# Kernel optimization log

Measured on AMD Instinct MI355X. Metric: run time of the kernel, lower is better.

## Reference

```python
import jax, jax.numpy as jnp
import numpy as np

IGNORE_INDEX = -100


def setup_inputs() -> dict:
    key = jax.random.key(0)
    k1, k2, k3 = jax.random.split(key, 3)
    BT, H, V = 2048, 2048, 128000
    x = jax.random.normal(k1, (BT, H), dtype=jnp.float32)
    weight = jax.random.normal(k2, (V, H), dtype=jnp.float32) * (1.0 / np.sqrt(H))
    target = jax.random.randint(k3, (BT,), 0, V, dtype=jnp.int64)
    return {"x": x, "weight": weight, "target": target}


def reference(x, weight, target):
    # Fused linear + cross-entropy forward (reduction='mean').
    # logits: [BT, V], accumulated in fp32 like the helion kernel.
    logits = jnp.einsum("bh,vh->bv", x.astype(jnp.float32), weight.astype(jnp.float32))
    lse = jax.nn.logsumexp(logits, axis=-1)  # [BT]
    target_logit = jnp.take_along_axis(logits, target[:, None], axis=-1)[:, 0]
    valid = (target != IGNORE_INDEX)
    nll = (lse - target_logit) * valid.astype(jnp.float32)  # [BT]
    n_non_ignore = valid.sum().astype(jnp.float32)
    loss = nll.sum() / n_non_ignore
    return loss.astype(x.dtype), lse
```

## Files before the change

kernel.cpp:

```cpp
#include <hip/hip_runtime.h>
#include <hip/hip_bf16.h>


typedef __bf16 bf16x8 __attribute__((ext_vector_type(8)));
typedef float f32x4  __attribute__((ext_vector_type(4)));
typedef float f32x16 __attribute__((ext_vector_type(16)));

#define BM 128
#define BN 128
#define BK 32
#define LDK 40

__device__ __forceinline__ unsigned pkbf(float a, float b) {
  __hip_bfloat162 h = __float22bfloat162_rn(float2{a, b});
  unsigned r;
  __builtin_memcpy(&r, &h, 4);
  return r;
}

__device__ __forceinline__ void gl16(const void* g, const void* l) {
  using GP = const unsigned __attribute__((address_space(1)))*;
  using LP = unsigned __attribute__((address_space(3)))*;
  __builtin_amdgcn_global_load_lds((GP)(unsigned long long)g,
                                   (LP)(unsigned)(unsigned long long)l, 16, 0, 0);
}

__global__ __launch_bounds__(256)
void k_cvt256(const float* __restrict__ src, __bf16* __restrict__ dst, int H, int NT)
{
  const int bid = blockIdx.x;
  const int kt = bid % NT;
  const int r = threadIdx.x;
  const float* s = src + (size_t)((bid / NT) * 256 + r) * H + kt * 64;
  __bf16* d = dst + (size_t)bid * 16384;
  #pragma unroll
  for (int j = 0; j < 8; ++j) {
    float4 f0 = ((const float4*)s)[2 * j];
    float4 f1 = ((const float4*)s)[2 * j + 1];
    uint4 p;
    p.x = pkbf(f0.x, f0.y); p.y = pkbf(f0.z, f0.w);
    p.z = pkbf(f1.x, f1.y); p.w = pkbf(f1.z, f1.w);
    *(uint4*)(d + (j >> 2) * 8192 + (j & 3) * 2048 + r * 8) = p;
  }
}

__global__ __launch_bounds__(256)
void k_tgt(const float* __restrict__ x, const float* __restrict__ w,
           const int* __restrict__ tgt, float* __restrict__ ws_t, int H)
{
  const int row  = blockIdx.x * 4 + (threadIdx.x >> 6);
  const int lane = threadIdx.x & 63;
  const int tv = tgt[row];
  if (tv == -100) { if (lane == 0) ws_t[row] = 0.f; return; }
  const float* xr = x + (size_t)row * H;
  const float* wr = w + (size_t)tv * H;
  float acc = 0.f;
  for (int j = lane * 4; j < H; j += 256) {
    float4 a = *(const float4*)(xr + j);
    float4 b = *(const float4*)(wr + j);
    acc += a.x * b.x + a.y * b.y + a.z * b.z + a.w * b.w;
  }
  #pragma unroll
  for (int m = 1; m < 64; m <<= 1) acc += __shfl_xor(acc, m, 64);
  if (lane == 0) ws_t[row] = acc;
}

#define VM4 asm volatile("s_waitcnt vmcnt(4)" ::: "memory");
#define VM0 asm volatile("s_waitcnt vmcnt(0)" ::: "memory");
#define NOVM
#define MEMFENCE asm volatile("" ::: "memory");

#define SLOT(SL, SLN, BCUR, BNXT, DO_ST, ST_S, DO_RA, VMW, DO_BAR)              \
  {                                                                             \
    _Pragma("unroll")                                                           \
    for (int m = 0; m < 4; ++m)                                                 \
      a1[m] = *(const bf16x8*)&As[SL][kcoff + (arow + (m + 4) * 16) * 8];       \
    __builtin_amdgcn_s_setprio(1);                                              \
    _Pragma("unroll")                                                           \
    for (int m = 0; m < 4; ++m)                                                 \
      _Pragma("unroll")                                                         \
      for (int n = 0; n < 4; ++n)                                               \
        acc[m][n] = __builtin_amdgcn_mfma_f32_16x16x32_bf16(a0[m], BCUR[n],     \
                                                            acc[m][n], 0, 0, 0);\
    __builtin_amdgcn_s_setprio(0);                                              \
    if (DO_ST) stage_slot(ST_S);                                                \
    VMW                                                                         \
    if (DO_BAR) { __builtin_amdgcn_s_barrier(); MEMFENCE }                      \
    if (DO_RA) {                                                                \
      _Pragma("unroll")                                                         \
      for (int m = 0; m < 4; ++m)                                               \
        a0[m] = *(const bf16x8*)&As[SLN][kcoff + (arow + m * 16) * 8];          \
      _Pragma("unroll")                                                         \
      for (int n = 0; n < 4; ++n)                                               \
        BNXT[n] = *(const bf16x8*)&Bs[SLN][kcoff + (bcol + n * 16) * 8];        \
    }                                                                           \
    __builtin_amdgcn_s_setprio(1);                                              \
    _Pragma("unroll")                                                           \
    for (int m = 0; m < 4; ++m)                                                 \
      _Pragma("unroll")                                                         \
      for (int n = 0; n < 4; ++n)                                               \
        acc[m + 4][n] = __builtin_amdgcn_mfma_f32_16x16x32_bf16(a1[m], BCUR[n], \
                                                         acc[m + 4][n], 0, 0, 0);\
    __builtin_amdgcn_s_setprio(0);                                              \
  }

__global__ __launch_bounds__(512, 2)
void k_gemm16(const __bf16* __restrict__ xb, const __bf16* __restrict__ wb,
              float* __restrict__ ws_m, float* __restrict__ ws_s,
              int NT, int NCB, int ROWB)
{
  __shared__ __bf16 As[4][8192];
  __shared__ __bf16 Bs[4][8192];

  int wg = blockIdx.x;
  const int nwg = gridDim.x;
  if ((nwg & 7) == 0) wg = (wg & 7) * (nwg >> 3) + (wg >> 3);
  const int rowb = wg % ROWB;
  const int cb   = wg / ROWB;
  const int row0 = rowb * 256;

  const int t    = threadIdx.x;
  const int lane = t & 63;
  const int wv   = t >> 6;
  const int wr   = wv >> 2;
  const int wc   = wv & 3;

  const int kcoff = (lane >> 4) * 2048;
  const int arow  = wr * 128 + (lane & 15);
  const int bcol  = wc * 64 + (lane & 15);

  const __bf16* ga = xb + (size_t)(rowb * NT) * 16384;
  const __bf16* gb = wb + (size_t)(cb * NT) * 16384;

  auto stage_slot = [&](int s) {
    const int ph = s & 3;
    const size_t off = (size_t)(s >> 1) * 16384 + (size_t)(s & 1) * 8192
                     + wv * 512 + lane * 8;
    const __bf16* a = ga + off;
    const __bf16* b = gb + off;
    gl16(a,        &As[ph][wv * 512]);
    gl16(a + 4096, &As[ph][4096 + wv * 512]);
    gl16(b,        &Bs[ph][wv * 512]);
    gl16(b + 4096, &Bs[ph][4096 + wv * 512]);
  };

  const int S = NT * 2;

  stage_slot(0); stage_slot(1);
  VM4
  __builtin_amdgcn_s_barrier();
  MEMFENCE

  f32x4 acc[8][4] = {};
  bf16x8 a0[4], a1[4], b0[4], b1[4];
  #pragma unroll
  for (int m = 0; m < 4; ++m)
    a0[m] = *(const bf16x8*)&As[0][kcoff + (arow + m * 16) * 8];
  #pragma unroll
  for (int n = 0; n < 4; ++n)
    b0[n] = *(const bf16x8*)&Bs[0][kcoff + (bcol + n * 16) * 8];

  for (int g = 0; g < (S - 4) / 4; ++g) {
    const int j0 = g * 4;
    SLOT(0, 1, b0, b1, true, j0 + 2, true, VM4, true)
    SLOT(1, 2, b1, b0, true, j0 + 3, true, VM4, true)
    SLOT(2, 3, b0, b1, true, j0 + 4, true, VM4, true)
    SLOT(3, 0, b1, b0, true, j0 + 5, true, VM4, true)
  }
  SLOT(0, 1, b0, b1, true,  S - 2, true,  VM4, true)
  SLOT(1, 2, b1, b0, true,  S - 1, true,  VM4, true)
  SLOT(2, 3, b0, b1, false, 0,     true,  VM0, true)
  SLOT(3, 0, b1, b0, false, 0,     false, NOVM, false)

  __syncthreads();

  float* redM = (float*)&As[0][0];
  float* redS = redM + 1024;
  const int g4 = (lane >> 4) * 4;
  #pragma unroll
  for (int m = 0; m < 8; ++m) {
    #pragma unroll
    for (int r = 0; r < 4; ++r) {
      const int rl = wr * 128 + m * 16 + g4 + r;
      float mx = fmaxf(fmaxf(acc[m][0][r], acc[m][1][r]),
                       fmaxf(acc[m][2][r], acc[m][3][r]));
      #pragma unroll
      for (int sh = 1; sh < 16; sh <<= 1) mx = fmaxf(mx, __shfl_xor(mx, sh, 64));
      float sv = 0.f;
      #pragma unroll
      for (int n = 0; n < 4; ++n) sv += expf(acc[m][n][r] - mx);
      #pragma unroll
      for (int sh = 1; sh < 16; sh <<= 1) sv += __shfl_xor(sv, sh, 64);
      if ((lane & 15) == 0) { redM[wc * 256 + rl] = mx; redS[wc * 256 + rl] = sv; }
    }
  }
  __syncthreads();
  if (t < 256) {
    const float m0 = redM[t], m1 = redM[256 + t], m2 = redM[512 + t], m3 = redM[768 + t];
    float M = fmaxf(fmaxf(m0, m1), fmaxf(m2, m3));
    float S2 = redS[t] * expf(m0 - M) + redS[256 + t] * expf(m1 - M)
             + redS[512 + t] * expf(m2 - M) + redS[768 + t] * expf(m3 - M);
    const int grow = row0 + t;
    ws_m[(size_t)grow * NCB + cb] = M;
    ws_s[(size_t)grow * NCB + cb] = S2;
  }
}

__global__ __launch_bounds__(256, 2)
void k_gemm_lse(const float* __restrict__ x, const float* __restrict__ w,
                const int* __restrict__ tgt,
                float* __restrict__ ws_m, float* __restrict__ ws_s,
                float* __restrict__ ws_t,
                int H, int NCB, int ROWB)
{
  __shared__ unsigned short As[2][BM * LDK];
  __shared__ unsigned short Bs[2][BN * LDK];

  const int bid  = blockIdx.x;
  const int rowb = bid % ROWB;
  const int cb   = bid / ROWB;
  const int row0 = rowb * BM;
  const int col0 = cb * BN;

  const int t    = threadIdx.x;
  const int lane = t & 63;
  const int wv   = t >> 6;
  const int sr = t >> 1;
  const int sk = (t & 1) * 16;

  const float* xa = x + (size_t)(row0 + sr) * H + sk;
  const float* wb = w + (size_t)(col0 + sr) * H + sk;

  float4 ra[4], rb[4];
  #pragma unroll
  for (int i = 0; i < 4; ++i) {
    ra[i] = *(const float4*)(xa + i * 4);
    rb[i] = *(const float4*)(wb + i * 4);
  }

  auto stage = [&](int buf) {
    uint4 p0, p1;
    p0.x = pkbf(ra[0].x, ra[0].y); p0.y = pkbf(ra[0].z, ra[0].w);
    p0.z = pkbf(ra[1].x, ra[1].y); p0.w = pkbf(ra[1].z, ra[1].w);
    p1.x = pkbf(ra[2].x, ra[2].y); p1.y = pkbf(ra[2].z, ra[2].w);
    p1.z = pkbf(ra[3].x, ra[3].y); p1.w = pkbf(ra[3].z, ra[3].w);
    *(uint4*)&As[buf][sr * LDK + sk]     = p0;
    *(uint4*)&As[buf][sr * LDK + sk + 8] = p1;
    p0.x = pkbf(rb[0].x, rb[0].y); p0.y = pkbf(rb[0].z, rb[0].w);
    p0.z = pkbf(rb[1].x, rb[1].y); p0.w = pkbf(rb[1].z, rb[1].w);
    p1.x = pkbf(rb[2].x, rb[2].y); p1.y = pkbf(rb[2].z, rb[2].w);
    p1.z = pkbf(rb[3].x, rb[3].y); p1.w = pkbf(rb[3].z, rb[3].w);
    *(uint4*)&Bs[buf][sr * LDK + sk]     = p0;
    *(uint4*)&Bs[buf][sr * LDK + sk + 8] = p1;
  };

  stage(0);
  __syncthreads();

  f32x16 acc[4] = {};
  const int rlo = lane & 31;
  const int hi  = lane >> 5;
  const int NT  = H / BK;
  int cur = 0;

  for (int kt = 0; kt < NT; ++kt) {
    const bool pf = (kt + 1 < NT);
    if (pf) {
      xa += BK; wb += BK;
      #pragma unroll
      for (int i = 0; i < 4; ++i) {
        ra[i] = *(const float4*)(xa + i * 4);
        rb[i] = *(const float4*)(wb + i * 4);
      }
    }
    const unsigned short* A = As[cur];
    const unsigned short* B = Bs[cur];
    #pragma unroll
    for (int ks = 0; ks < 2; ++ks) {
      const int koff = ks * 16 + hi * 8;
      bf16x8 a = *(const bf16x8*)&A[(wv * 32 + rlo) * LDK + koff];
      #pragma unroll
      for (int nf = 0; nf < 4; ++nf) {
        bf16x8 b = *(const bf16x8*)&B[(nf * 32 + rlo) * LDK + koff];
        acc[nf] = __builtin_amdgcn_mfma_f32_32x32x16_bf16(a, b, acc[nf], 0, 0, 0);
      }
    }
    if (pf) stage(cur ^ 1);
    __syncthreads();
    cur ^= 1;
  }

  #pragma unroll
  for (int reg = 0; reg < 16; ++reg) {
    const int row = wv * 32 + (reg & 3) + 8 * (reg >> 2) + 4 * hi;
    float mx = fmaxf(fmaxf(acc[0][reg], acc[1][reg]), fmaxf(acc[2][reg], acc[3][reg]));
    #pragma unroll
    for (int m = 1; m < 32; m <<= 1) mx = fmaxf(mx, __shfl_xor(mx, m, 64));
    float s = 0.f;
    #pragma unroll
    for (int nf = 0; nf < 4; ++nf) s += expf(acc[nf][reg] - mx);
    #pragma unroll
    for (int m = 1; m < 32; m <<= 1) s += __shfl_xor(s, m, 64);
    const int grow = row0 + row;
    if (rlo == 0) {
      ws_m[(size_t)grow * NCB + cb] = mx;
      ws_s[(size_t)grow * NCB + cb] = s;
    }
    const int tv = tgt[grow];
    #pragma unroll
    for (int nf = 0; nf < 4; ++nf) {
      if (tv == col0 + nf * 32 + rlo) ws_t[grow] = acc[nf][reg];
    }
  }
}

__global__ void k_rowlse(const float* __restrict__ ws_m, const float* __restrict__ ws_s,
                         const float* __restrict__ ws_t, const int* __restrict__ tgt,
                         float* __restrict__ out, float* __restrict__ ws_nll, int NCB)
{
  const int row = blockIdx.x;
  const int t = threadIdx.x;
  const float* pm = ws_m + (size_t)row * NCB;
  const float* ps = ws_s + (size_t)row * NCB;
  __shared__ float red[8];

  float M = -3.0e38f;
  for (int j = t; j < NCB; j += 256) M = fmaxf(M, pm[j]);
  #pragma unroll
  for (int m = 1; m < 64; m <<= 1) M = fmaxf(M, __shfl_xor(M, m, 64));
  if ((t & 63) == 0) red[t >> 6] = M;
  __syncthreads();
  M = fmaxf(fmaxf(red[0], red[1]), fmaxf(red[2], red[3]));

  float S = 0.f;
  for (int j = t; j < NCB; j += 256) S += ps[j] * expf(pm[j] - M);
  #pragma unroll
  for (int m = 1; m < 64; m <<= 1) S += __shfl_xor(S, m, 64);
  if ((t & 63) == 0) red[4 + (t >> 6)] = S;
  __syncthreads();

  if (t == 0) {
    S = red[4] + red[5] + red[6] + red[7];
    const float lse = M + logf(S);
    out[1 + row] = lse;
    const int tv = tgt[row];
    ws_nll[row] = (tv != -100) ? (lse - ws_t[row]) : 0.f;
  }
}

__global__ void k_loss(const float* __restrict__ ws_nll, const int* __restrict__ tgt,
                       float* __restrict__ out, int BT)
{
  const int t = threadIdx.x;
  float s = 0.f, c = 0.f;
  for (int i = t; i < BT; i += 256) {
    s += ws_nll[i];
    c += (tgt[i] != -100) ? 1.f : 0.f;
  }
  __shared__ float rs[4], rc[4];
  #pragma unroll
  for (int m = 1; m < 64; m <<= 1) { s += __shfl_xor(s, m, 64); c += __shfl_xor(c, m, 64); }
  if ((t & 63) == 0) { rs[t >> 6] = s; rc[t >> 6] = c; }
  __syncthreads();
  if (t == 0) {
    s = rs[0] + rs[1] + rs[2] + rs[3];
    c = rc[0] + rc[1] + rc[2] + rc[3];
    out[0] = s / c;
  }
}

extern "C" void kernel_launch(void* const* d_in, const int* in_sizes, int n_in,
                              void* d_out, int out_size, void* d_ws, size_t ws_size,
                              hipStream_t stream)
{
  const float* x  = (const float*)d_in[0];
  const float* w  = (const float*)d_in[1];
  const int* tgt  = (const int*)d_in[2];
  float* out      = (float*)d_out;

  const int BT = in_sizes[2];
  const int H  = in_sizes[0] / BT;
  const int V  = in_sizes[1] / H;

  const int NT    = H / 64;
  const int ROWB  = BT / 256;
  const int NCB   = V / 256;

  const size_t bf_elems   = (size_t)BT * H + (size_t)V * H;
  const size_t need_bytes = bf_elems * 2 + ((size_t)2 * BT * NCB + 2 * (size_t)BT) * 4;

  if (ws_size >= need_bytes && (BT % 256) == 0 && (V % 256) == 0 && (H % 128) == 0) {
    __bf16* x_bf = (__bf16*)d_ws;
    __bf16* w_bf = x_bf + (size_t)BT * H;
    float* ws_m   = (float*)(w_bf + (size_t)V * H);
    float* ws_s   = ws_m + (size_t)BT * NCB;
    float* ws_t   = ws_s + (size_t)BT * NCB;
    float* ws_nll = ws_t + BT;

    k_cvt256<<<(V / 256) * NT, 256, 0, stream>>>(w, w_bf, H, NT);
    k_cvt256<<<(BT / 256) * NT, 256, 0, stream>>>(x, x_bf, H, NT);
    k_tgt<<<BT / 4, 256, 0, stream>>>(x, w, tgt, ws_t, H);
    k_gemm16<<<ROWB * NCB, 512, 0, stream>>>(x_bf, w_bf, ws_m, ws_s, NT, NCB, ROWB);
    k_rowlse<<<BT, 256, 0, stream>>>(ws_m, ws_s, ws_t, tgt, out, ws_nll, NCB);
    k_loss<<<1, 256, 0, stream>>>(ws_nll, tgt, out, BT);
  } else {
    const int ROWB1 = BT / BM;
    const int NCB1  = V / BN;
    float* ws_m   = (float*)d_ws;
    float* ws_s   = ws_m + (size_t)BT * NCB1;
    float* ws_t   = ws_s + (size_t)BT * NCB1;
    float* ws_nll = ws_t + BT;

    k_gemm_lse<<<ROWB1 * NCB1, 256, 0, stream>>>(x, w, tgt, ws_m, ws_s, ws_t, H, NCB1, ROWB1);
    k_rowlse<<<BT, 256, 0, stream>>>(ws_m, ws_s, ws_t, tgt, out, ws_nll, NCB1);
    k_loss<<<1, 256, 0, stream>>>(ws_nll, tgt, out, BT);
  }
}
```

Before: 1.307 ms.

## Add 128x128-tile bf16 GEMM path with 3-stage LDS pipeline as default

Measured after the change: 1.441 ms. 10.3% more time.

```diff
diff --git a/kernel.cpp b/kernel.cpp
--- a/kernel.cpp
+++ b/kernel.cpp
@@ -23,6 +23,32 @@
   using LP = unsigned __attribute__((address_space(3)))*;
   __builtin_amdgcn_global_load_lds((GP)(unsigned long long)g,
                                    (LP)(unsigned)(unsigned long long)l, 16, 0, 0);
+}
+
+#define VM4 asm volatile("s_waitcnt vmcnt(4)" ::: "memory");
+#define VM0 asm volatile("s_waitcnt vmcnt(0)" ::: "memory");
+#define MEMFENCE asm volatile("" ::: "memory");
+
+__global__ __launch_bounds__(256)
+void k_cvt_tile(const float* __restrict__ src, __bf16* __restrict__ dst, int H, int NT)
+{
+  const int bid = blockIdx.x;
+  const int kt = bid % NT;
+  const int t = threadIdx.x;
+  const int r = t >> 1, hh = (t & 1) * 16;
+  const float* s = src + (size_t)((bid / NT) * 128 + r) * H + kt * 32 + hh;
+  float4 f0 = ((const float4*)s)[0];
+  float4 f1 = ((const float4*)s)[1];
+  float4 f2 = ((const float4*)s)[2];
+  float4 f3 = ((const float4*)s)[3];
+  uint4 p0, p1;
+  p0.x = pkbf(f0.x, f0.y); p0.y = pkbf(f0.z, f0.w);
+  p0.z = pkbf(f1.x, f1.y); p0.w = pkbf(f1.z, f1.w);
+  p1.x = pkbf(f2.x, f2.y); p1.y = pkbf(f2.z, f2.w);
+  p1.z = pkbf(f3.x, f3.y); p1.w = pkbf(f3.z, f3.w);
+  __bf16* d = dst + (size_t)bid * 4096 + ((t & 1) * 2) * 1024 + r * 8;
+  *(uint4*)d = p0;
+  *(uint4*)(d + 1024) = p1;
 }
 
 __global__ __launch_bounds__(256)
@@ -65,12 +91,119 @@
   if (lane == 0) ws_t[row] = acc;
 }
 
-#define VM4 asm volatile("s_waitcnt vmcnt(4)" ::: "memory");
-#define VM0 asm volatile("s_waitcnt vmcnt(0)" ::: "memory");
-#define NOVM
-#define MEMFENCE asm volatile("" ::: "memory");
-
-#define SLOT(SL, SLN, BCUR, BNXT, DO_ST, ST_S, DO_RA, VMW, DO_BAR)              \
+__global__ __launch_bounds__(256, 3)
+void k_gemm128(const __bf16* __restrict__ xb, const __bf16* __restrict__ wb,
+               float* __restrict__ ws_m, float* __restrict__ ws_s,
+               int S, int NCB, int ROWB)
+{
+  __shared__ __bf16 As[3][4096];
+  __shared__ __bf16 Bs[3][4096];
+
+  int wg = blockIdx.x;
+  const int nwg = gridDim.x;
+  if ((nwg & 7) == 0) wg = (wg & 7) * (nwg >> 3) + (wg >> 3);
+  const int rowb = wg % ROWB;
+  const int cb   = wg / ROWB;
+  const int row0 = rowb * 128;
+
+  const int t    = threadIdx.x;
+  const int lane = t & 63;
+  const int wv   = t >> 6;
+  const int wr   = wv >> 1;
+  const int wc   = wv & 1;
+
+  const int kcoff = (lane >> 4) * 1024;
+  const int arow  = wr * 64 + (lane & 15);
+  const int bcol  = wc * 64 + (lane & 15);
+
+  const __bf16* ga = xb + (size_t)(rowb * S) * 4096;
+  const __bf16* gb = wb + (size_t)(cb * S) * 4096;
+
+  auto stage_slot = [&](int s, int r) {
+    const size_t off = (size_t)s * 4096 + wv * 512 + lane * 8;
+    const __bf16* a = ga + off;
+    const __bf16* b = gb + off;
+    gl16(a,        &As[r][wv * 512]);
+    gl16(a + 2048, &As[r][2048 + wv * 512]);
+    gl16(b,        &Bs[r][wv * 512]);
+    gl16(b + 2048, &Bs[r][2048 + wv * 512]);
+  };
+
+  stage_slot(0, 0);
+  stage_slot(1, 1);
+  VM4
+  __builtin_amdgcn_s_barrier();
+  MEMFENCE
+
+  f32x4 acc[4][4] = {};
+  bf16x8 aC[4], bC[4];
+  #pragma unroll
+  for (int m = 0; m < 4; ++m)
+    aC[m] = *(const bf16x8*)&As[0][kcoff + (arow + m * 16) * 8];
+  #pragma unroll
+  for (int n = 0; n < 4; ++n)
+    bC[n] = *(const bf16x8*)&Bs[0][kcoff + (bcol + n * 16) * 8];
+
+  int r0 = 0, r1 = 1, r2 = 2;
+  for (int j = 0; j < S; ++j) {
+    if (j + 2 < S) stage_slot(j + 2, r2);
+    __builtin_amdgcn_s_setprio(1);
+    #pragma unroll
+    for (int m = 0; m < 4; ++m)
+      #pragma unroll
+      for (int n = 0; n < 4; ++n)
+        acc[m][n] = __builtin_amdgcn_mfma_f32_16x16x32_bf16(aC[m], bC[n],
+                                                            acc[m][n], 0, 0, 0);
+    __builtin_amdgcn_s_setprio(0);
+    if (j + 2 < S)      { VM4 }
+    else if (j + 1 < S) { VM0 }
+    __builtin_amdgcn_s_barrier();
+    MEMFENCE
+    if (j + 1 < S) {
+      #pragma unroll
+      for (int m = 0; m < 4; ++m)
+        aC[m] = *(const bf16x8*)&As[r1][kcoff + (arow + m * 16) * 8];
+      #pragma unroll
+      for (int n = 0; n < 4; ++n)
+        bC[n] = *(const bf16x8*)&Bs[r1][kcoff + (bcol + n * 16) * 8];
+    }
+    const int tmp = r0; r0 = r1; r1 = r2; r2 = tmp;
+  }
+
+  __syncthreads();
+
+  float* redM = (float*)&As[0][0];
+  float* redS = redM + 256;
+  const int g4 = (lane >> 4) * 4;
+  #pragma unroll
+  for (int m = 0; m < 4; ++m) {
+    #pragma unroll
+    for (int r = 0; r < 4; ++r) {
+      const int rl = wr * 64 + m * 16 + g4 + r;
+      float mx = fmaxf(fmaxf(acc[m][0][r], acc[m][1][r]),
+                       fmaxf(acc[m][2][r], acc[m][3][r]));
+      #pragma unroll
+      for (int sh = 1; sh < 16; sh <<= 1) mx = fmaxf(mx, __shfl_xor(mx, sh, 64));
+      float sv = 0.f;
+      #pragma unroll
+      for (int n = 0; n < 4; ++n) sv += expf(acc[m][n][r] - mx);
+      #pragma unroll
+      for (int sh = 1; sh < 16; sh <<= 1) sv += __shfl_xor(sv, sh, 64);
+      if ((lane & 15) == 0) { redM[wc * 128 + rl] = mx; redS[wc * 128 + rl] = sv; }
+    }
+  }
+  __syncthreads();
+  if (t < 128) {
+    const float m0 = redM[t], m1 = redM[128 + t];
+    const float M = fmaxf(m0, m1);
+    const float Ss = redS[t] * expf(m0 - M) + redS[128 + t] * expf(m1 - M);
+    const int grow = row0 + t;
+    ws_m[(size_t)grow * NCB + cb] = M;
+    ws_s[(size_t)grow * NCB + cb] = Ss;
+  }
+}
+
+#define SLOT9(SL, SLN, BCUR, BNXT, DO_ST, ST_S, DO_RA, VMW, DO_BAR)             \
   {                                                                             \
     _Pragma("unroll")                                                           \
     for (int m = 0; m < 4; ++m)                                                 \
@@ -103,6 +236,8 @@
                                                          acc[m + 4][n], 0, 0, 0);\
     __builtin_amdgcn_s_setprio(0);                                              \
   }
+#define VM8 asm volatile("s_waitcnt vmcnt(8)" ::: "memory");
+#define NOVM
 
 __global__ __launch_bounds__(512, 2)
 void k_gemm16(const __bf16* __restrict__ xb, const __bf16* __restrict__ wb,
@@ -162,15 +297,15 @@
 
   for (int g = 0; g < (S - 4) / 4; ++g) {
     const int j0 = g * 4;
-    SLOT(0, 1, b0, b1, true, j0 + 2, true, VM4, true)
-    SLOT(1, 2, b1, b0, true, j0 + 3, true, VM4, true)
-    SLOT(2, 3, b0, b1, true, j0 + 4, true, VM4, true)
-    SLOT(3, 0, b1, b0, true, j0 + 5, true, VM4, true)
-  }
-  SLOT(0, 1, b0, b1, true,  S - 2, true,  VM4, true)
-  SLOT(1, 2, b1, b0, true,  S - 1, true,  VM4, true)
-  SLOT(2, 3, b0, b1, false, 0,     true,  VM0, true)
-  SLOT(3, 0, b1, b0, false, 0,     false, NOVM, false)
+    SLOT9(0, 1, b0, b1, true, j0 + 2, true, VM4, true)
+    SLOT9(1, 2, b1, b0, true, j0 + 3, true, VM4, true)
+    SLOT9(2, 3, b0, b1, true, j0 + 4, true, VM4, true)
+    SLOT9(3, 0, b1, b0, true, j0 + 5, true, VM4, true)
+  }
+  SLOT9(0, 1, b0, b1, true,  S - 2, true,  VM4, true)
+  SLOT9(1, 2, b1, b0, true,  S - 1, true,  VM4, true)
+  SLOT9(2, 3, b0, b1, false, 0,     true,  VM0, true)
+  SLOT9(3, 0, b1, b0, false, 0,     false, NOVM, false)
 
   __syncthreads();
 
@@ -382,26 +517,47 @@
   const int H  = in_sizes[0] / BT;
   const int V  = in_sizes[1] / H;
 
-  const int NT    = H / 64;
-  const int ROWB  = BT / 256;
-  const int NCB   = V / 256;
-
-  const size_t bf_elems   = (size_t)BT * H + (size_t)V * H;
-  const size_t need_bytes = bf_elems * 2 + ((size_t)2 * BT * NCB + 2 * (size_t)BT) * 4;
-
-  if (ws_size >= need_bytes && (BT % 256) == 0 && (V % 256) == 0 && (H % 128) == 0) {
+  const size_t bf_elems = (size_t)BT * H + (size_t)V * H;
+
+  const int S128    = H / 32;
+  const int ROWB128 = BT / 128;
+  const int NCB128  = V / 128;
+  const size_t needA = bf_elems * 2 + ((size_t)2 * BT * NCB128 + 2 * (size_t)BT) * 4;
+
+  const int NT256   = H / 64;
+  const int ROWB256 = BT / 256;
+  const int NCB256  = V / 256;
+  const size_t needB = bf_elems * 2 + ((size_t)2 * BT * NCB256 + 2 * (size_t)BT) * 4;
+
+  if (ws_size >= needA && (BT % 256) == 0 && (V % 256) == 0 && (H % 128) == 0) {
     __bf16* x_bf = (__bf16*)d_ws;
     __bf16* w_bf = x_bf + (size_t)BT * H;
     float* ws_m   = (float*)(w_bf + (size_t)V * H);
-    float* ws_s   = ws_m + (size_t)BT * NCB;
-    float* ws_t   = ws_s + (size_t)BT * NCB;
+    float* ws_s   = ws_m + (size_t)BT * NCB128;
+    float* ws_t   = ws_s + (size_t)BT * NCB128;
     float* ws_nll = ws_t + BT;
 
-    k_cvt256<<<(V / 256) * NT, 256, 0, stream>>>(w, w_bf, H, NT);
-    k_cvt256<<<(BT / 256) * NT, 256, 0, stream>>>(x, x_bf, H, NT);
+    k_cvt_tile<<<(V / 128) * S128, 256, 0, stream>>>(w, w_bf, H, S128);
+    k_cvt_tile<<<(BT / 128) * S128, 256, 0, stream>>>(x, x_bf, H, S128);
     k_tgt<<<BT / 4, 256, 0, stream>>>(x, w, tgt, ws_t, H);
-    k_gemm16<<<ROWB * NCB, 512, 0, stream>>>(x_bf, w_bf, ws_m, ws_s, NT, NCB, ROWB);
-    k_rowlse<<<BT, 256, 0, stream>>>(ws_m, ws_s, ws_t, tgt, out, ws_nll, NCB);
+    k_gemm128<<<ROWB128 * NCB128, 256, 0, stream>>>(x_bf, w_bf, ws_m, ws_s,
+                                                    S128, NCB128, ROWB128);
+    k_rowlse<<<BT, 256, 0, stream>>>(ws_m, ws_s, ws_t, tgt, out, ws_nll, NCB128);
+    k_loss<<<1, 256, 0, stream>>>(ws_nll, tgt, out, BT);
+  } else if (ws_size >= needB && (BT % 256) == 0 && (V % 256) == 0 && (H % 128) == 0) {
+    __bf16* x_bf = (__bf16*)d_ws;
+    __bf16* w_bf = x_bf + (size_t)BT * H;
+    float* ws_m   = (float*)(w_bf + (size_t)V * H);
+    float* ws_s   = ws_m + (size_t)BT * NCB256;
+    float* ws_t   = ws_s + (size_t)BT * NCB256;
+    float* ws_nll = ws_t + BT;
+
+    k_cvt256<<<(V / 256) * NT256, 256, 0, stream>>>(w, w_bf, H, NT256);
+    k_cvt256<<<(BT / 256) * NT256, 256, 0, stream>>>(x, x_bf, H, NT256);
+    k_tgt<<<BT / 4, 256, 0, stream>>>(x, w, tgt, ws_t, H);
+    k_gemm16<<<ROWB256 * NCB256, 512, 0, stream>>>(x_bf, w_bf, ws_m, ws_s,
+                                                   NT256, NCB256, ROWB256);
+    k_rowlse<<<BT, 256, 0, stream>>>(ws_m, ws_s, ws_t, tgt, out, ws_nll, NCB256);
     k_loss<<<1, 256, 0, stream>>>(ws_nll, tgt, out, BT);
   } else {
     const int ROWB1 = BT / BM;
```

## Split GEMM block work across 16 waves with a simpler staged loop

Applied to the files above, without the earlier changes.

Result: no change. 1.320 ms (+1.0%).

```diff
diff --git a/kernel.cpp b/kernel.cpp
--- a/kernel.cpp
+++ b/kernel.cpp
@@ -24,6 +24,10 @@
   __builtin_amdgcn_global_load_lds((GP)(unsigned long long)g,
                                    (LP)(unsigned)(unsigned long long)l, 16, 0, 0);
 }
+
+#define VM2 asm volatile("s_waitcnt vmcnt(2)" ::: "memory");
+#define VM0 asm volatile("s_waitcnt vmcnt(0)" ::: "memory");
+#define MEMFENCE asm volatile("" ::: "memory");
 
 __global__ __launch_bounds__(256)
 void k_cvt256(const float* __restrict__ src, __bf16* __restrict__ dst, int H, int NT)
@@ -65,49 +69,10 @@
   if (lane == 0) ws_t[row] = acc;
 }
 
-#define VM4 asm volatile("s_waitcnt vmcnt(4)" ::: "memory");
-#define VM0 asm volatile("s_waitcnt vmcnt(0)" ::: "memory");
-#define NOVM
-#define MEMFENCE asm volatile("" ::: "memory");
-
-#define SLOT(SL, SLN, BCUR, BNXT, DO_ST, ST_S, DO_RA, VMW, DO_BAR)              \
-  {                                                                             \
-    _Pragma("unroll")                                                           \
-    for (int m = 0; m < 4; ++m)                                                 \
-      a1[m] = *(const bf16x8*)&As[SL][kcoff + (arow + (m + 4) * 16) * 8];       \
-    __builtin_amdgcn_s_setprio(1);                                              \
-    _Pragma("unroll")                                                           \
-    for (int m = 0; m < 4; ++m)                                                 \
-      _Pragma("unroll")                                                         \
-      for (int n = 0; n < 4; ++n)                                               \
-        acc[m][n] = __builtin_amdgcn_mfma_f32_16x16x32_bf16(a0[m], BCUR[n],     \
-                                                            acc[m][n], 0, 0, 0);\
-    __builtin_amdgcn_s_setprio(0);                                              \
-    if (DO_ST) stage_slot(ST_S);                                                \
-    VMW                                                                         \
-    if (DO_BAR) { __builtin_amdgcn_s_barrier(); MEMFENCE }                      \
-    if (DO_RA) {                                                                \
-      _Pragma("unroll")                                                         \
-      for (int m = 0; m < 4; ++m)                                               \
-        a0[m] = *(const bf16x8*)&As[SLN][kcoff + (arow + m * 16) * 8];          \
-      _Pragma("unroll")                                                         \
-      for (int n = 0; n < 4; ++n)                                               \
-        BNXT[n] = *(const bf16x8*)&Bs[SLN][kcoff + (bcol + n * 16) * 8];        \
-    }                                                                           \
-    __builtin_amdgcn_s_setprio(1);                                              \
-    _Pragma("unroll")                                                           \
-    for (int m = 0; m < 4; ++m)                                                 \
-      _Pragma("unroll")                                                         \
-      for (int n = 0; n < 4; ++n)                                               \
-        acc[m + 4][n] = __builtin_amdgcn_mfma_f32_16x16x32_bf16(a1[m], BCUR[n], \
-                                                         acc[m + 4][n], 0, 0, 0);\
-    __builtin_amdgcn_s_setprio(0);                                              \
-  }
-
-__global__ __launch_bounds__(512, 2)
-void k_gemm16(const __bf16* __restrict__ xb, const __bf16* __restrict__ wb,
-              float* __restrict__ ws_m, float* __restrict__ ws_s,
-              int NT, int NCB, int ROWB)
+__global__ __launch_bounds__(1024, 4)
+void k_gemm1024(const __bf16* __restrict__ xb, const __bf16* __restrict__ wb,
+                float* __restrict__ ws_m, float* __restrict__ ws_s,
+                int S, int NCB, int ROWB)
 {
   __shared__ __bf16 As[4][8192];
   __shared__ __bf16 Bs[4][8192];
@@ -126,51 +91,49 @@
   const int wc   = wv & 3;
 
   const int kcoff = (lane >> 4) * 2048;
-  const int arow  = wr * 128 + (lane & 15);
+  const int arow  = wr * 64 + (lane & 15);
   const int bcol  = wc * 64 + (lane & 15);
 
-  const __bf16* ga = xb + (size_t)(rowb * NT) * 16384;
-  const __bf16* gb = wb + (size_t)(cb * NT) * 16384;
-
-  auto stage_slot = [&](int s) {
-    const int ph = s & 3;
+  const __bf16* ga = xb + (size_t)(rowb * S / 2) * 16384;
+  const __bf16* gb = wb + (size_t)(cb * S / 2) * 16384;
+
+  auto stage_slot = [&](int s, int r) {
     const size_t off = (size_t)(s >> 1) * 16384 + (size_t)(s & 1) * 8192
                      + wv * 512 + lane * 8;
-    const __bf16* a = ga + off;
-    const __bf16* b = gb + off;
-    gl16(a,        &As[ph][wv * 512]);
-    gl16(a + 4096, &As[ph][4096 + wv * 512]);
-    gl16(b,        &Bs[ph][wv * 512]);
-    gl16(b + 4096, &Bs[ph][4096 + wv * 512]);
+    gl16(ga + off, &As[r][wv * 512]);
+    gl16(gb + off, &Bs[r][wv * 512]);
   };
 
-  const int S = NT * 2;
-
-  stage_slot(0); stage_slot(1);
-  VM4
+  stage_slot(0, 0);
+  stage_slot(1, 1);
+  VM2
   __builtin_amdgcn_s_barrier();
   MEMFENCE
 
-  f32x4 acc[8][4] = {};
-  bf16x8 a0[4], a1[4], b0[4], b1[4];
-  #pragma unroll
-  for (int m = 0; m < 4; ++m)
-    a0[m] = *(const bf16x8*)&As[0][kcoff + (arow + m * 16) * 8];
-  #pragma unroll
-  for (int n = 0; n < 4; ++n)
-    b0[n] = *(const bf16x8*)&Bs[0][kcoff + (bcol + n * 16) * 8];
-
-  for (int g = 0; g < (S - 4) / 4; ++g) {
-    const int j0 = g * 4;
-    SLOT(0, 1, b0, b1, true, j0 + 2, true, VM4, true)
-    SLOT(1, 2, b1, b0, true, j0 + 3, true, VM4, true)
-    SLOT(2, 3, b0, b1, true, j0 + 4, true, VM4, true)
-    SLOT(3, 0, b1, b0, true, j0 + 5, true, VM4, true)
-  }
-  SLOT(0, 1, b0, b1, true,  S - 2, true,  VM4, true)
-  SLOT(1, 2, b1, b0, true,  S - 1, true,  VM4, true)
-  SLOT(2, 3, b0, b1, false, 0,     true,  VM0, true)
-  SLOT(3, 0, b1, b0, false, 0,     false, NOVM, false)
+  f32x4 acc[4][4] = {};
+
+  for (int j = 0; j < S; ++j) {
+    const int rj = j & 3;
+    if (j + 2 < S) stage_slot(j + 2, (j + 2) & 3);
+    bf16x8 aC[4], bC[4];
+    #pragma unroll
+    for (int m = 0; m < 4; ++m)
+      aC[m] = *(const bf16x8*)&As[rj][kcoff + (arow + m * 16) * 8];
+    #pragma unroll
+    for (int n = 0; n < 4; ++n)
+      bC[n] = *(const bf16x8*)&Bs[rj][kcoff + (bcol + n * 16) * 8];
+    __builtin_amdgcn_s_setprio(1);
+    #pragma unroll
+    for (int m = 0; m < 4; ++m)
+      #pragma unroll
+      for (int n = 0; n < 4; ++n)
+        acc[m][n] = __builtin_amdgcn_mfma_f32_16x16x32_bf16(aC[m], bC[n],
+                                                            acc[m][n], 0, 0, 0);
+    __builtin_amdgcn_s_setprio(0);
+    if (j + 2 < S)      { VM2 }
+    else if (j + 1 < S) { VM0 }
+    if (j + 1 < S) { __builtin_amdgcn_s_barrier(); MEMFENCE }
+  }
 
   __syncthreads();
 
@@ -178,10 +141,10 @@
   float* redS = redM + 1024;
   const int g4 = (lane >> 4) * 4;
   #pragma unroll
-  for (int m = 0; m < 8; ++m) {
+  for (int m = 0; m < 4; ++m) {
     #pragma unroll
     for (int r = 0; r < 4; ++r) {
-      const int rl = wr * 128 + m * 16 + g4 + r;
+      const int rl = wr * 64 + m * 16 + g4 + r;
       float mx = fmaxf(fmaxf(acc[m][0][r], acc[m][1][r]),
                        fmaxf(acc[m][2][r], acc[m][3][r]));
       #pragma unroll
@@ -400,7 +363,8 @@
     k_cvt256<<<(V / 256) * NT, 256, 0, stream>>>(w, w_bf, H, NT);
     k_cvt256<<<(BT / 256) * NT, 256, 0, stream>>>(x, x_bf, H, NT);
     k_tgt<<<BT / 4, 256, 0, stream>>>(x, w, tgt, ws_t, H);
-    k_gemm16<<<ROWB * NCB, 512, 0, stream>>>(x_bf, w_bf, ws_m, ws_s, NT, NCB, ROWB);
+    k_gemm1024<<<ROWB * NCB, 1024, 0, stream>>>(x_bf, w_bf, ws_m, ws_s,
+                                                NT * 2, NCB, ROWB);
     k_rowlse<<<BT, 256, 0, stream>>>(ws_m, ws_s, ws_t, tgt, out, ws_nll, NCB);
     k_loss<<<1, 256, 0, stream>>>(ws_nll, tgt, out, BT);
   } else {
```
